# Performance work log

Measured on AMD Instinct MI355X. Metric: run time of the kernel, lower is better.

## Reference

```python
import jax, jax.numpy as jnp
import numpy as np

B, S, D, H = 2, 2048, 1024, 16
DK = D // H


def setup_inputs() -> dict:
    key = jax.random.key(0)
    ks = jax.random.split(key, 10)
    scale = 1.0 / np.sqrt(D)
    x = jax.random.normal(ks[0], (B, S, D), dtype=jnp.float32)
    # causal mask: 1 = attend, 0 = masked (module's create_causal_mask)
    mask = jnp.tril(jnp.ones((S, S), dtype=jnp.int32))[None, None]
    Wq = jax.random.normal(ks[1], (D, D), jnp.float32) * scale
    bq = jax.random.normal(ks[2], (D,), jnp.float32) * 0.01
    Wk = jax.random.normal(ks[3], (D, D), jnp.float32) * scale
    bk = jax.random.normal(ks[4], (D,), jnp.float32) * 0.01
    Wv = jax.random.normal(ks[5], (D, D), jnp.float32) * scale
    bv = jax.random.normal(ks[6], (D,), jnp.float32) * 0.01
    Wo = jax.random.normal(ks[7], (D, D), jnp.float32) * scale
    bo = jax.random.normal(ks[8], (D,), jnp.float32) * 0.01
    return {"x": x, "mask": mask, "Wq": Wq, "bq": bq, "Wk": Wk, "bk": bk,
            "Wv": Wv, "bv": bv, "Wo": Wo, "bo": bo}


def reference(x, mask, Wq, bq, Wk, bk, Wv, bv, Wo, bo):
    b, s, _ = x.shape
    # projections; [B,S,D] -> [B,H,S,DK]
    def split_heads(t):
        return t.reshape(b, s, H, DK).transpose(0, 2, 1, 3)
    Q = split_heads(x @ Wq + bq)
    K = split_heads(x @ Wk + bk)
    V = split_heads(x @ Wv + bv)
    scores = jnp.einsum('bhqd,bhkd->bhqk', Q, K) / np.sqrt(DK)
    scores = jnp.where(mask == 0, jnp.float32(-1e9), scores)
    attn = jax.nn.softmax(scores, axis=-1)  # dropout p=0 -> identity
    ctx = jnp.einsum('bhqk,bhkd->bhqd', attn, V)
    ctx = ctx.transpose(0, 2, 1, 3).reshape(b, s, D)
    return ctx @ Wo + bo
```

## Files before the change

kernel.cpp:

```cpp
#include <hip/hip_runtime.h>
#include <hip/hip_bf16.h>


typedef _Float16 f16x8 __attribute__((ext_vector_type(8)));
typedef _Float16 f16x4 __attribute__((ext_vector_type(4)));
typedef _Float16 f16x2 __attribute__((ext_vector_type(2)));
typedef float f32x4 __attribute__((ext_vector_type(4)));

#define QSCALE 0.180336880111112f

__device__ __forceinline__ void async_copy16(const _Float16* gsrc,
                                             _Float16* ldst) {
  __builtin_amdgcn_global_load_lds(
      (const __attribute__((address_space(1))) void*)gsrc,
      (__attribute__((address_space(3))) void*)ldst, 16, 0, 0);
}

__global__ __launch_bounds__(256) void prep(
    const float* __restrict__ x, _Float16* __restrict__ xh,
    const float* __restrict__ W0, const float* __restrict__ W1,
    const float* __restrict__ W2, const float* __restrict__ W3,
    _Float16* __restrict__ T0, _Float16* __restrict__ T1,
    _Float16* __restrict__ T2, _Float16* __restrict__ T3) {
  if (blockIdx.x < 4096) {
    int i = (blockIdx.x * 256 + threadIdx.x) * 4;
    float4 v = *(const float4*)(x + i);
    f16x4 o;
    o.x = (_Float16)v.x; o.y = (_Float16)v.y;
    o.z = (_Float16)v.z; o.w = (_Float16)v.w;
    *(f16x4*)(xh + i) = o;
    return;
  }
  const int id = blockIdx.x - 4096;
  const int w = id >> 10, rem = id & 1023;
  const int bx = rem & 31, by = rem >> 5;
  const float* W; _Float16* T;
  switch (w) {
    case 0: W = W0; T = T0; break;
    case 1: W = W1; T = T1; break;
    case 2: W = W2; T = T2; break;
    default: W = W3; T = T3; break;
  }
  __shared__ _Float16 tile[32][33];
  const int tx = threadIdx.x & 31, ty = threadIdx.x >> 5;
  const int n0 = bx * 32, k0 = by * 32;
  for (int i = 0; i < 4; i++) {
    int kk = k0 + ty + i * 8;
    tile[ty + i * 8][tx] = (_Float16)W[(size_t)kk * 1024 + n0 + tx];
  }
  __syncthreads();
  for (int i = 0; i < 4; i++) {
    int nn = n0 + ty + i * 8;
    T[(size_t)nn * 1024 + k0 + tx] = tile[tx][ty + i * 8];
  }
}

__global__ __launch_bounds__(256) void gemm_qkv(
    const _Float16* __restrict__ A, const _Float16* __restrict__ BtAll,
    const float* __restrict__ bq, const float* __restrict__ bk,
    const float* __restrict__ bv, _Float16* __restrict__ Qh,
    _Float16* __restrict__ Kh, _Float16* __restrict__ VT) {
  __shared__ _Float16 As[128 * 32];
  __shared__ _Float16 Bs[128 * 32];
  __shared__ _Float16 tbuf[64 * 136];
  const int tid = threadIdx.x;
  const int wave = tid >> 6, lane = tid & 63;
  const int lr = lane & 15, lq = lane >> 4;
  const int m0 = blockIdx.x * 128, n0 = blockIdx.y * 128;
  const int rw = (wave & 1) * 64, cw = (wave >> 1) * 64;

  const int sel = blockIdx.y >> 3;
  const float* bias = sel == 0 ? bq : (sel == 1 ? bk : bv);
  const int c0 = n0 & 1023;

  f32x4 acc[4][4] = {};
  const int r0 = wave * 32 + (lane >> 2);
  const int woff = (lane & 3) * 8;

  for (int kt = 0; kt < 1024; kt += 32) {
    __syncthreads();
    async_copy16(A + (size_t)(m0 + r0) * 1024 + kt + woff, As + r0 * 32 + woff);
    async_copy16(A + (size_t)(m0 + r0 + 16) * 1024 + kt + woff,
                 As + (r0 + 16) * 32 + woff);
    async_copy16(BtAll + (size_t)(n0 + r0) * 1024 + kt + woff,
                 Bs + r0 * 32 + woff);
    async_copy16(BtAll + (size_t)(n0 + r0 + 16) * 1024 + kt + woff,
                 Bs + (r0 + 16) * 32 + woff);
    __syncthreads();
    f16x8 af[4], bf[4];
    for (int i = 0; i < 4; i++)
      af[i] = *(const f16x8*)(As + (rw + i * 16 + lr) * 32 + lq * 8);
    for (int j = 0; j < 4; j++)
      bf[j] = *(const f16x8*)(Bs + (cw + j * 16 + lr) * 32 + lq * 8);
    for (int i = 0; i < 4; i++)
      for (int j = 0; j < 4; j++)
        acc[i][j] = __builtin_amdgcn_mfma_f32_16x16x32_f16(af[i], bf[j],
                                                           acc[i][j], 0, 0, 0);
  }

  if (sel == 2) {
    const int bb = m0 >> 11, ss0 = m0 & 2047;
    const int cs = tid & 15, dkr = tid >> 4;
    for (int jj = 0; jj < 2; jj++) {
      __syncthreads();
      if ((wave >> 1) == jj) {
        for (int i = 0; i < 4; i++) {
          const int sl = rw + i * 16 + lq * 4;
          for (int j = 0; j < 4; j++) {
            const int dk = j * 16 + lr;
            const float bvl = bias[c0 + jj * 64 + dk];
            f16x4 pv;
            for (int r = 0; r < 4; r++) pv[r] = (_Float16)(acc[i][j][r] + bvl);
            *(f16x4*)(tbuf + dk * 136 + sl) = pv;
          }
        }
      }
      __syncthreads();
      const int hh = (c0 + jj * 64) >> 6;
      _Float16* dst = VT + ((size_t)(bb * 16 + hh) * 64) * 2048 + ss0;
      for (int k = 0; k < 4; k++) {
        const int dk = dkr + k * 16;
        *(uint4*)(dst + (size_t)dk * 2048 + cs * 8) =
            *(const uint4*)(tbuf + dk * 136 + cs * 8);
      }
    }
  } else {
    _Float16* out = sel == 0 ? Qh : Kh;
    const float scl = sel == 0 ? QSCALE : 1.0f;
    for (int i = 0; i < 4; i++) {
      const int row = m0 + rw + i * 16 + lq * 4;
      for (int j = 0; j < 4; j++) {
        const int col = c0 + cw + j * 16 + lr;
        const float bvl = bias[col];
        for (int r = 0; r < 4; r++)
          out[(size_t)(row + r) * 1024 + col] =
              (_Float16)((acc[i][j][r] + bvl) * scl);
      }
    }
  }
}

__global__ __launch_bounds__(256) void gemm_out(
    const _Float16* __restrict__ A, const _Float16* __restrict__ Bt,
    const float* __restrict__ bias, float* __restrict__ out) {
  __shared__ _Float16 As[128 * 32];
  __shared__ _Float16 Bs[64 * 32];
  const int tid = threadIdx.x;
  const int wave = tid >> 6, lane = tid & 63;
  const int lr = lane & 15, lq = lane >> 4;
  const int m0 = blockIdx.x * 128, n0 = blockIdx.y * 64;
  const int rw = (wave & 1) * 64, cw = (wave >> 1) * 32;
  f32x4 acc[4][2] = {};
  const int r0 = wave * 32 + (lane >> 2);
  const int br = tid >> 2;
  const int woff = (lane & 3) * 8;

  for (int kt = 0; kt < 1024; kt += 32) {
    __syncthreads();
    async_copy16(A + (size_t)(m0 + r0) * 1024 + kt + woff, As + r0 * 32 + woff);
    async_copy16(A + (size_t)(m0 + r0 + 16) * 1024 + kt + woff,
                 As + (r0 + 16) * 32 + woff);
    async_copy16(Bt + (size_t)(n0 + br) * 1024 + kt + woff,
                 Bs + br * 32 + woff);
    __syncthreads();
    f16x8 af[4], bf[2];
    for (int i = 0; i < 4; i++)
      af[i] = *(const f16x8*)(As + (rw + i * 16 + lr) * 32 + lq * 8);
    for (int j = 0; j < 2; j++)
      bf[j] = *(const f16x8*)(Bs + (cw + j * 16 + lr) * 32 + lq * 8);
    for (int i = 0; i < 4; i++)
      for (int j = 0; j < 2; j++)
        acc[i][j] = __builtin_amdgcn_mfma_f32_16x16x32_f16(af[i], bf[j],
                                                           acc[i][j], 0, 0, 0);
  }
  for (int i = 0; i < 4; i++) {
    const int row = m0 + rw + i * 16 + lq * 4;
    for (int j = 0; j < 2; j++) {
      const int col = n0 + cw + j * 16 + lr;
      const float bvl = bias[col];
      for (int r = 0; r < 4; r++)
        out[(size_t)(row + r) * 1024 + col] = acc[i][j][r] + bvl;
    }
  }
}

__global__ __launch_bounds__(512, 4) void attn(const _Float16* __restrict__ Q,
                                               const _Float16* __restrict__ K,
                                               const _Float16* __restrict__ VT,
                                               _Float16* __restrict__ ctx) {
  const int sp = blockIdx.y;
  const int bh = blockIdx.x;
  const int b = bh >> 4, h = bh & 15;
  const int tid = threadIdx.x, wave = tid >> 6, lane = tid & 63;
  const int lr = lane & 15, lq = lane >> 4;
  const int rg = wave & 3;
  const int kvh = wave >> 2;
  const int kho = kvh * 32;
  const size_t qkbase = ((size_t)b * 2048) * 1024 + h * 64;
  const size_t vtbase = ((size_t)bh) * 64 * 2048;

  __shared__ _Float16 Ks[2][64 * 72];
  __shared__ _Float16 Vs[2][64 * 72];
  __shared__ float cb[4 * 64 * 24];

  f16x4 onesf;
  {
    _Float16 ov = (lr == 0) ? (_Float16)1.0f : (_Float16)0.0f;
    for (int i = 0; i < 4; i++) onesf[i] = ov;
  }

  const int sgr = tid >> 3, sgc = (tid & 7) * 8;
  const _Float16* Kg0 = K + qkbase + (size_t)sgr * 1024 + sgc;
  const _Float16* Vg0 = VT + vtbase + (size_t)sgr * 2048 + sgc;

  for (int ph = 0; ph < 2; ph++) {
    const int st = ph ? 31 - sp : sp;
    const int qmin = st * 64 + rg * 16;
    const _Float16* qp = Q + qkbase + (size_t)(qmin + lr) * 1024 + lq * 8;
    f16x8 qf0 = *(const f16x8*)qp;
    f16x8 qf1 = *(const f16x8*)(qp + 32);
    f32x4 o[4] = {};
    f32x4 ol = {};
    uint4 ka = *(const uint4*)Kg0;
    uint4 va = *(const uint4*)Vg0;

    for (int t = 0; t <= st; t++) {
      _Float16* ksb = Ks[t & 1];
      _Float16* vsb = Vs[t & 1];
      *(uint4*)(ksb + sgr * 72 + sgc) = ka;
      *(uint4*)(vsb + sgr * 72 + sgc) = va;
      __syncthreads();
      if (t < st) {
        const _Float16* kg = Kg0 + (size_t)(t + 1) * 64 * 1024;
        const _Float16* vg = Vg0 + (t + 1) * 64;
        ka = *(const uint4*)kg;
        va = *(const uint4*)vg;
      }
      const int kvw = t * 64 + kho;
      if (kvw > qmin + 15) continue;

      f32x4 s[2];
      for (int ksl = 0; ksl < 2; ksl++) {
        const int ksg = kvh * 2 + ksl;
        f16x8 k0 = *(const f16x8*)(ksb + (ksg * 16 + lr) * 72 + lq * 8);
        f16x8 k1 = *(const f16x8*)(ksb + (ksg * 16 + lr) * 72 + 32 + lq * 8);
        f32x4 z = {};
        z = __builtin_amdgcn_mfma_f32_16x16x32_f16(k0, qf0, z, 0, 0, 0);
        z = __builtin_amdgcn_mfma_f32_16x16x32_f16(k1, qf1, z, 0, 0, 0);
        s[ksl] = z;
      }
      if (kvw + 31 > qmin) {
        const int qcol = qmin + lr;
        for (int ksl = 0; ksl < 2; ksl++)
          for (int r = 0; r < 4; r++)
            if (kvw + ksl * 16 + lq * 4 + r > qcol) s[ksl][r] = -1e30f;
      }
      f16x4 pa[2];
      for (int ksl = 0; ksl < 2; ksl++) {
        float p0 = exp2f(s[ksl][0]);
        float p1 = exp2f(s[ksl][1]);
        float p2 = exp2f(s[ksl][2]);
        float p3 = exp2f(s[ksl][3]);
        f16x2 q01 =
            __builtin_bit_cast(f16x2, __builtin_amdgcn_cvt_pkrtz(p0, p1));
        f16x2 q23 =
            __builtin_bit_cast(f16x2, __builtin_amdgcn_cvt_pkrtz(p2, p3));
        pa[ksl] = __builtin_shufflevector(q01, q23, 0, 1, 2, 3);
      }
      __builtin_amdgcn_s_setprio(1);
      for (int ksl = 0; ksl < 2; ksl++) {
        const int ksg = kvh * 2 + ksl;
        for (int dn = 0; dn < 4; dn++) {
          f16x4 vf =
              *(const f16x4*)(vsb + (dn * 16 + lr) * 72 + ksg * 16 + lq * 4);
          o[dn] = __builtin_amdgcn_mfma_f32_16x16x16f16(pa[ksl], vf, o[dn], 0,
                                                        0, 0);
        }
        ol = __builtin_amdgcn_mfma_f32_16x16x16f16(pa[ksl], onesf, ol, 0, 0, 0);
      }
      __builtin_amdgcn_s_setprio(0);
    }

    __syncthreads();
    if (wave >= 4) {
      float* p = cb + ((wave - 4) * 64 + lane) * 24;
      *(f32x4*)(p + 0) = o[0];
      *(f32x4*)(p + 4) = o[1];
      *(f32x4*)(p + 8) = o[2];
      *(f32x4*)(p + 12) = o[3];
      *(f32x4*)(p + 16) = ol;
    }
    __syncthreads();
    if (wave < 4) {
      const float* p = cb + (wave * 64 + lane) * 24;
      o[0] += *(const f32x4*)(p + 0);
      o[1] += *(const f32x4*)(p + 4);
      o[2] += *(const f32x4*)(p + 8);
      o[3] += *(const f32x4*)(p + 12);
      ol += *(const f32x4*)(p + 16);
      for (int r = 0; r < 4; r++) {
        float lv = __shfl(ol[r], lane & 48);
        float inv = 1.0f / lv;
        const int row = qmin + lq * 4 + r;
        for (int dn = 0; dn < 4; dn++)
          ctx[qkbase + (size_t)row * 1024 + dn * 16 + lr] =
              (_Float16)(o[dn][r] * inv);
      }
    }
  }
}

extern "C" void kernel_launch(void* const* d_in, const int* in_sizes, int n_in,
                              void* d_out, int out_size, void* d_ws,
                              size_t ws_size, hipStream_t stream) {
  const float* x  = (const float*)d_in[0];
  const float* Wq = (const float*)d_in[2];
  const float* bq = (const float*)d_in[3];
  const float* Wk = (const float*)d_in[4];
  const float* bk = (const float*)d_in[5];
  const float* Wv = (const float*)d_in[6];
  const float* bv = (const float*)d_in[7];
  const float* Wo = (const float*)d_in[8];
  const float* bo = (const float*)d_in[9];
  float* out = (float*)d_out;

  char* ws = (char*)d_ws;
  const size_t MB = 1 << 20;
  _Float16* xh  = (_Float16*)(ws);
  _Float16* WTs = (_Float16*)(ws + 8 * MB);
  _Float16* WqT = WTs;
  _Float16* WkT = (_Float16*)(ws + 10 * MB);
  _Float16* WvT = (_Float16*)(ws + 12 * MB);
  _Float16* WoT = (_Float16*)(ws + 14 * MB);
  _Float16* Qh  = (_Float16*)(ws + 16 * MB);
  _Float16* Kh  = (_Float16*)(ws + 24 * MB);
  _Float16* VT  = (_Float16*)(ws + 32 * MB);
  _Float16* ctx = (_Float16*)(ws);

  prep<<<8192, 256, 0, stream>>>(x, xh, Wq, Wk, Wv, Wo, WqT, WkT, WvT, WoT);
  gemm_qkv<<<dim3(32, 24), 256, 0, stream>>>(xh, WTs, bq, bk, bv, Qh, Kh, VT);
  attn<<<dim3(32, 16), 512, 0, stream>>>(Qh, Kh, VT, ctx);
  gemm_out<<<dim3(32, 16), 256, 0, stream>>>(ctx, WoT, bo, out);
}
```

Measured before the change: 189.8 us.

## Drop LDS staging in attention; waves load K/V fragments directly from global

Reorganizes the attention kernel so each wave owns 32 query rows and a 16-key slice of each 64-key tile. Waves load their K and V^T fragments straight from global memory into registers, with K prefetched one tile ahead, instead of staging tiles through double-buffered shared memory. This removes the per-tile __syncthreads and LDS traffic, and each wave skips tiles lying fully above the causal diagonal. In exchange, partial results are now reduced across four key-slice waves in two LDS rounds, and K/V global reads are duplicated across waves, relying on cache hits.

```diff
diff --git a/kernel.cpp b/kernel.cpp
--- a/kernel.cpp
+++ b/kernel.cpp
@@ -193,15 +193,13 @@
   const int b = bh >> 4, h = bh & 15;
   const int tid = threadIdx.x, wave = tid >> 6, lane = tid & 63;
   const int lr = lane & 15, lq = lane >> 4;
-  const int rg = wave & 3;
-  const int kvh = wave >> 2;
-  const int kho = kvh * 32;
+  const int rg = wave & 1;
+  const int kvq = wave >> 1;
+  const int kho = kvq * 16;
   const size_t qkbase = ((size_t)b * 2048) * 1024 + h * 64;
   const size_t vtbase = ((size_t)bh) * 64 * 2048;
 
-  __shared__ _Float16 Ks[2][64 * 72];
-  __shared__ _Float16 Vs[2][64 * 72];
-  __shared__ float cb[4 * 64 * 24];
+  __shared__ float cb[4 * 64 * 44];
 
   f16x4 onesf;
   {
@@ -209,102 +207,140 @@
     for (int i = 0; i < 4; i++) onesf[i] = ov;
   }
 
-  const int sgr = tid >> 3, sgc = (tid & 7) * 8;
-  const _Float16* Kg0 = K + qkbase + (size_t)sgr * 1024 + sgc;
-  const _Float16* Vg0 = VT + vtbase + (size_t)sgr * 2048 + sgc;
+  const _Float16* Kg = K + qkbase + (size_t)(kho + lr) * 1024 + lq * 8;
+  const _Float16* Vg = VT + vtbase + (size_t)lr * 2048 + kho + lq * 4;
 
   for (int ph = 0; ph < 2; ph++) {
     const int st = ph ? 31 - sp : sp;
-    const int qmin = st * 64 + rg * 16;
+    const int qmin = st * 64 + rg * 32;
     const _Float16* qp = Q + qkbase + (size_t)(qmin + lr) * 1024 + lq * 8;
-    f16x8 qf0 = *(const f16x8*)qp;
-    f16x8 qf1 = *(const f16x8*)(qp + 32);
-    f32x4 o[4] = {};
-    f32x4 ol = {};
-    uint4 ka = *(const uint4*)Kg0;
-    uint4 va = *(const uint4*)Vg0;
-
-    for (int t = 0; t <= st; t++) {
-      _Float16* ksb = Ks[t & 1];
-      _Float16* vsb = Vs[t & 1];
-      *(uint4*)(ksb + sgr * 72 + sgc) = ka;
-      *(uint4*)(vsb + sgr * 72 + sgc) = va;
-      __syncthreads();
-      if (t < st) {
-        const _Float16* kg = Kg0 + (size_t)(t + 1) * 64 * 1024;
-        const _Float16* vg = Vg0 + (t + 1) * 64;
-        ka = *(const uint4*)kg;
-        va = *(const uint4*)vg;
-      }
+    f16x8 qA0 = *(const f16x8*)qp;
+    f16x8 qA1 = *(const f16x8*)(qp + 32);
+    f16x8 qB0 = *(const f16x8*)(qp + (size_t)16 * 1024);
+    f16x8 qB1 = *(const f16x8*)(qp + (size_t)16 * 1024 + 32);
+
+    f32x4 oA[4] = {}, oB[4] = {};
+    f32x4 olA = {}, olB = {};
+
+    const int num = qmin + 31 - kho;
+    const int tmaxw = num >= 0 ? (num >> 6) : -1;
+
+    f16x8 k0c = *(const f16x8*)Kg;
+    f16x8 k1c = *(const f16x8*)(Kg + 32);
+
+    for (int t = 0; t <= tmaxw; t++) {
+      const _Float16* vb = Vg + t * 64;
+      f16x4 v0 = *(const f16x4*)(vb);
+      f16x4 v1 = *(const f16x4*)(vb + 32768);
+      f16x4 v2 = *(const f16x4*)(vb + 65536);
+      f16x4 v3 = *(const f16x4*)(vb + 98304);
+      f16x8 k0n, k1n;
+      if (t < tmaxw) {
+        const _Float16* kp = Kg + (size_t)(t + 1) * 65536;
+        k0n = *(const f16x8*)kp;
+        k1n = *(const f16x8*)(kp + 32);
+      }
+
+      f32x4 sA = {}, sB = {};
+      sA = __builtin_amdgcn_mfma_f32_16x16x32_f16(k0c, qA0, sA, 0, 0, 0);
+      sA = __builtin_amdgcn_mfma_f32_16x16x32_f16(k1c, qA1, sA, 0, 0, 0);
+      sB = __builtin_amdgcn_mfma_f32_16x16x32_f16(k0c, qB0, sB, 0, 0, 0);
+      sB = __builtin_amdgcn_mfma_f32_16x16x32_f16(k1c, qB1, sB, 0, 0, 0);
+
       const int kvw = t * 64 + kho;
-      if (kvw > qmin + 15) continue;
-
-      f32x4 s[2];
-      for (int ksl = 0; ksl < 2; ksl++) {
-        const int ksg = kvh * 2 + ksl;
-        f16x8 k0 = *(const f16x8*)(ksb + (ksg * 16 + lr) * 72 + lq * 8);
-        f16x8 k1 = *(const f16x8*)(ksb + (ksg * 16 + lr) * 72 + 32 + lq * 8);
-        f32x4 z = {};
-        z = __builtin_amdgcn_mfma_f32_16x16x32_f16(k0, qf0, z, 0, 0, 0);
-        z = __builtin_amdgcn_mfma_f32_16x16x32_f16(k1, qf1, z, 0, 0, 0);
-        s[ksl] = z;
-      }
-      if (kvw + 31 > qmin) {
+      if (kvw + 15 > qmin) {
         const int qcol = qmin + lr;
-        for (int ksl = 0; ksl < 2; ksl++)
-          for (int r = 0; r < 4; r++)
-            if (kvw + ksl * 16 + lq * 4 + r > qcol) s[ksl][r] = -1e30f;
-      }
-      f16x4 pa[2];
-      for (int ksl = 0; ksl < 2; ksl++) {
-        float p0 = exp2f(s[ksl][0]);
-        float p1 = exp2f(s[ksl][1]);
-        float p2 = exp2f(s[ksl][2]);
-        float p3 = exp2f(s[ksl][3]);
+        for (int r = 0; r < 4; r++)
+          if (kvw + lq * 4 + r > qcol) sA[r] = -1e30f;
+      }
+      if (kvw + 15 > qmin + 16) {
+        const int qcol = qmin + 16 + lr;
+        for (int r = 0; r < 4; r++)
+          if (kvw + lq * 4 + r > qcol) sB[r] = -1e30f;
+      }
+
+      f16x4 paA, paB;
+      {
+        float p0 = exp2f(sA[0]), p1 = exp2f(sA[1]);
+        float p2 = exp2f(sA[2]), p3 = exp2f(sA[3]);
         f16x2 q01 =
             __builtin_bit_cast(f16x2, __builtin_amdgcn_cvt_pkrtz(p0, p1));
         f16x2 q23 =
             __builtin_bit_cast(f16x2, __builtin_amdgcn_cvt_pkrtz(p2, p3));
-        pa[ksl] = __builtin_shufflevector(q01, q23, 0, 1, 2, 3);
-      }
+        paA = __builtin_shufflevector(q01, q23, 0, 1, 2, 3);
+      }
+      {
+        float p0 = exp2f(sB[0]), p1 = exp2f(sB[1]);
+        float p2 = exp2f(sB[2]), p3 = exp2f(sB[3]);
+        f16x2 q01 =
+            __builtin_bit_cast(f16x2, __builtin_amdgcn_cvt_pkrtz(p0, p1));
+        f16x2 q23 =
+            __builtin_bit_cast(f16x2, __builtin_amdgcn_cvt_pkrtz(p2, p3));
+        paB = __builtin_shufflevector(q01, q23, 0, 1, 2, 3);
+      }
+
       __builtin_amdgcn_s_setprio(1);
-      for (int ksl = 0; ksl < 2; ksl++) {
-        const int ksg = kvh * 2 + ksl;
-        for (int dn = 0; dn < 4; dn++) {
-          f16x4 vf =
-              *(const f16x4*)(vsb + (dn * 16 + lr) * 72 + ksg * 16 + lq * 4);
-          o[dn] = __builtin_amdgcn_mfma_f32_16x16x16f16(pa[ksl], vf, o[dn], 0,
-                                                        0, 0);
-        }
-        ol = __builtin_amdgcn_mfma_f32_16x16x16f16(pa[ksl], onesf, ol, 0, 0, 0);
-      }
+      oA[0] = __builtin_amdgcn_mfma_f32_16x16x16f16(paA, v0, oA[0], 0, 0, 0);
+      oA[1] = __builtin_amdgcn_mfma_f32_16x16x16f16(paA, v1, oA[1], 0, 0, 0);
+      oA[2] = __builtin_amdgcn_mfma_f32_16x16x16f16(paA, v2, oA[2], 0, 0, 0);
+      oA[3] = __builtin_amdgcn_mfma_f32_16x16x16f16(paA, v3, oA[3], 0, 0, 0);
+      oB[0] = __builtin_amdgcn_mfma_f32_16x16x16f16(paB, v0, oB[0], 0, 0, 0);
+      oB[1] = __builtin_amdgcn_mfma_f32_16x16x16f16(paB, v1, oB[1], 0, 0, 0);
+      oB[2] = __builtin_amdgcn_mfma_f32_16x16x16f16(paB, v2, oB[2], 0, 0, 0);
+      oB[3] = __builtin_amdgcn_mfma_f32_16x16x16f16(paB, v3, oB[3], 0, 0, 0);
+      olA = __builtin_amdgcn_mfma_f32_16x16x16f16(paA, onesf, olA, 0, 0, 0);
+      olB = __builtin_amdgcn_mfma_f32_16x16x16f16(paB, onesf, olB, 0, 0, 0);
       __builtin_amdgcn_s_setprio(0);
-    }
-
-    __syncthreads();
-    if (wave >= 4) {
-      float* p = cb + ((wave - 4) * 64 + lane) * 24;
-      *(f32x4*)(p + 0) = o[0];
-      *(f32x4*)(p + 4) = o[1];
-      *(f32x4*)(p + 8) = o[2];
-      *(f32x4*)(p + 12) = o[3];
-      *(f32x4*)(p + 16) = ol;
-    }
-    __syncthreads();
-    if (wave < 4) {
-      const float* p = cb + (wave * 64 + lane) * 24;
-      o[0] += *(const f32x4*)(p + 0);
-      o[1] += *(const f32x4*)(p + 4);
-      o[2] += *(const f32x4*)(p + 8);
-      o[3] += *(const f32x4*)(p + 12);
-      ol += *(const f32x4*)(p + 16);
+
+      if (t < tmaxw) { k0c = k0n; k1c = k1n; }
+    }
+
+    __syncthreads();
+    if (kvq == 1 || kvq == 3) {
+      float* p = cb + (((kvq == 1 ? 0 : 2) + rg) * 64 + lane) * 44;
+      *(f32x4*)(p + 0) = oA[0];  *(f32x4*)(p + 4) = oA[1];
+      *(f32x4*)(p + 8) = oA[2];  *(f32x4*)(p + 12) = oA[3];
+      *(f32x4*)(p + 16) = oB[0]; *(f32x4*)(p + 20) = oB[1];
+      *(f32x4*)(p + 24) = oB[2]; *(f32x4*)(p + 28) = oB[3];
+      *(f32x4*)(p + 32) = olA;   *(f32x4*)(p + 36) = olB;
+    }
+    __syncthreads();
+    if (kvq == 0 || kvq == 2) {
+      float* p = cb + (((kvq == 0 ? 0 : 2) + rg) * 64 + lane) * 44;
+      oA[0] += *(const f32x4*)(p + 0);  oA[1] += *(const f32x4*)(p + 4);
+      oA[2] += *(const f32x4*)(p + 8);  oA[3] += *(const f32x4*)(p + 12);
+      oB[0] += *(const f32x4*)(p + 16); oB[1] += *(const f32x4*)(p + 20);
+      oB[2] += *(const f32x4*)(p + 24); oB[3] += *(const f32x4*)(p + 28);
+      olA += *(const f32x4*)(p + 32);   olB += *(const f32x4*)(p + 36);
+      if (kvq == 2) {
+        *(f32x4*)(p + 0) = oA[0];  *(f32x4*)(p + 4) = oA[1];
+        *(f32x4*)(p + 8) = oA[2];  *(f32x4*)(p + 12) = oA[3];
+        *(f32x4*)(p + 16) = oB[0]; *(f32x4*)(p + 20) = oB[1];
+        *(f32x4*)(p + 24) = oB[2]; *(f32x4*)(p + 28) = oB[3];
+        *(f32x4*)(p + 32) = olA;   *(f32x4*)(p + 36) = olB;
+      }
+    }
+    __syncthreads();
+    if (kvq == 0) {
+      const float* p = cb + ((2 + rg) * 64 + lane) * 44;
+      oA[0] += *(const f32x4*)(p + 0);  oA[1] += *(const f32x4*)(p + 4);
+      oA[2] += *(const f32x4*)(p + 8);  oA[3] += *(const f32x4*)(p + 12);
+      oB[0] += *(const f32x4*)(p + 16); oB[1] += *(const f32x4*)(p + 20);
+      oB[2] += *(const f32x4*)(p + 24); oB[3] += *(const f32x4*)(p + 28);
+      olA += *(const f32x4*)(p + 32);   olB += *(const f32x4*)(p + 36);
       for (int r = 0; r < 4; r++) {
-        float lv = __shfl(ol[r], lane & 48);
-        float inv = 1.0f / lv;
-        const int row = qmin + lq * 4 + r;
+        float lvA = __shfl(olA[r], lane & 48);
+        float invA = 1.0f / lvA;
+        const int rowA = qmin + lq * 4 + r;
         for (int dn = 0; dn < 4; dn++)
-          ctx[qkbase + (size_t)row * 1024 + dn * 16 + lr] =
-              (_Float16)(o[dn][r] * inv);
+          ctx[qkbase + (size_t)rowA * 1024 + dn * 16 + lr] =
+              (_Float16)(oA[dn][r] * invA);
+        float lvB = __shfl(olB[r], lane & 48);
+        float invB = 1.0f / lvB;
+        const int rowB = qmin + 16 + lq * 4 + r;
+        for (int dn = 0; dn < 4; dn++)
+          ctx[qkbase + (size_t)rowB * 1024 + dn * 16 + lr] =
+              (_Float16)(oB[dn][r] * invB);
       }
     }
   }
```

Result: slower. 247.0 us (+30.2%).
